# Performance work log

Measured on AMD Instinct MI355X. Metric: run time of the kernel, lower is better.

Reference implementation:

```python
import jax, jax.numpy as jnp
from jax import lax
import numpy as np

GB_MAX = 3      # BandEst guard-band upper bound
RB = 1          # refer_band
PAD = RB + 1    # refer_band + init_guard_band(1)
N_OFF = 16      # ring offsets: kernel (4,4) -> N=16
BN_EPS = 1e-5

def _ring_offsets():
    idx = np.arange(-PAD, PAD + 1)
    X, Y = np.meshgrid(idx, idx, indexing='ij')
    hp = wp = 2 * PAD + 1
    def ring(M):
        return np.concatenate([M[0:RB, 0:wp - RB].ravel(), M[0:hp - RB, wp - RB:wp].ravel(),
                               M[hp - RB:hp, RB:wp].ravel(), M[RB:hp, 0:RB].ravel()])
    return ring(X).astype(np.float32), ring(Y).astype(np.float32)

PRF_X, PRF_Y = _ring_offsets()
BLOCK = np.repeat(np.arange(4), N_OFF // 4)  # offset n -> direction block (top,right,bottom,left)


def q_shift(x, H, W, shift=1, gamma=0.25):
    B, T, C = x.shape
    img = x.transpose(0, 2, 1).reshape(B, C, H, W)
    g = int(C * gamma)
    out = jnp.zeros_like(img)
    out = out.at[:, 0:g, :, shift:].set(img[:, 0:g, :, :W - shift])
    out = out.at[:, g:2 * g, :, :W - shift].set(img[:, g:2 * g, :, shift:])
    out = out.at[:, 2 * g:3 * g, shift:, :].set(img[:, 2 * g:3 * g, :H - shift, :])
    out = out.at[:, 3 * g:4 * g, :H - shift, :].set(img[:, 3 * g:4 * g, shift:, :])
    out = out.at[:, 4 * g:].set(img[:, 4 * g:])
    return out.reshape(B, C, T).transpose(0, 2, 1)


def bi_wkv(w, u, k, v):
    # Bi-directional WKV: y_t = (sum_{i<t} e^{-(t-1-i)w + k_i} v_i + e^{u+k_t} v_t
    #                            + sum_{i>t} e^{-(i-1-t)w + k_i} v_i) / (same with v->1)
    B, T, C = k.shape
    kT = k.transpose(1, 0, 2)
    vT = v.transpose(1, 0, 2)

    def step(carry, kv):
        m, a, b = carry  # state represents e^m * (a, b): (sum exp, weighted v)
        kt, vt = kv
        out = (m, a, b)  # exclusive prefix (excludes current token)
        m2 = jnp.maximum(m - w, kt)
        e1 = jnp.exp(m - w - m2)
        e2 = jnp.exp(kt - m2)
        return (m2, e1 * a + e2, e1 * b + e2 * vt), out

    init = (jnp.full((B, C), -1e38, k.dtype), jnp.zeros((B, C), k.dtype), jnp.zeros((B, C), k.dtype))
    _, (mf, af, bf) = lax.scan(step, init, (kT, vT))
    _, (mb, ab, bb) = lax.scan(step, init, (kT[::-1], vT[::-1]))
    mb, ab, bb = mb[::-1], ab[::-1], bb[::-1]
    ms = u + kT
    M = jnp.maximum(jnp.maximum(mf, mb), ms)
    ef, eb, es = jnp.exp(mf - M), jnp.exp(mb - M), jnp.exp(ms - M)
    num = ef * bf + eb * bb + es * vT
    den = ef * af + eb * ab + es
    return (num / den).transpose(1, 0, 2)


def band_est(x, cvw, cvb, bns_v, bnb_v, chw, chb, bns_h, bnb_h):
    dn = ('NCHW', 'OIHW', 'NCHW')
    gv = lax.conv_general_dilated(x, cvw, (1, 1), ((GB_MAX, GB_MAX), (0, 0)), dimension_numbers=dn) + cvb[None, :, None, None]
    gh = lax.conv_general_dilated(x, chw, (1, 1), ((0, 0), (GB_MAX, GB_MAX)), dimension_numbers=dn) + chb[None, :, None, None]
    inv = np.float32(1.0 / np.sqrt(1.0 + BN_EPS))  # eval BN: running mean 0, var 1
    gv = gv * (bns_v * inv)[None, :, None, None] + bnb_v[None, :, None, None]
    gh = gh * (bns_h * inv)[None, :, None, None] + bnb_h[None, :, None, None]
    return jnp.concatenate([jax.nn.sigmoid(gv), jax.nn.sigmoid(gh)], 1) * (GB_MAX - 1)


def _gather(xp_flat, ix, iy, wp, h, w):
    b, c = xp_flat.shape[0], xp_flat.shape[1]
    idx = (ix * wp + iy).reshape(b, 1, -1)
    return jnp.take_along_axis(xp_flat, idx, axis=2).reshape(b, c, h, w, N_OFF)


def ada_peak(x_img, cvw, cvb, bns_v, bnb_v, chw, chb, bns_h, bnb_h):
    b, c, h, w = x_img.shape
    xp = jnp.pad(x_img, ((0, 0), (0, 0), (PAD, PAD), (PAD, PAD)), mode='edge')
    hp, wp = h + 2 * PAD, w + 2 * PAD
    xp_flat = xp.reshape(b, c, hp * wp)
    gb = band_est(x_img, cvw, cvb, bns_v, bnb_v, chw, chb, bns_h, bnb_h)  # (b,4,h,w)
    zero = jnp.zeros_like(gb[:, 0])
    mvx = jnp.stack([-gb[:, 0], zero, gb[:, 1], zero], -1)  # (b,h,w,4) per block
    mvy = jnp.stack([zero, gb[:, 3], zero, -gb[:, 2]], -1)
    move_x = mvx[..., BLOCK]  # (b,h,w,16)
    move_y = mvy[..., BLOCK]
    cx = jnp.arange(PAD, h + PAD, dtype=x_img.dtype)
    cy = jnp.arange(PAD, w + PAD, dtype=x_img.dtype)
    px = cx[None, :, None, None] + jnp.asarray(PRF_X)[None, None, None, :] + move_x
    py = cy[None, None, :, None] + jnp.asarray(PRF_Y)[None, None, None, :] + move_y
    flx = jnp.floor(lax.stop_gradient(px))
    fly = jnp.floor(lax.stop_gradient(py))
    q_lt_x = jnp.clip(flx, 0, hp - 1)
    q_lt_y = jnp.clip(fly, 0, wp - 1)
    q_rb_x = jnp.clip(flx + 1, 0, hp - 1)
    q_rb_y = jnp.clip(fly + 1, 0, wp - 1)
    pxc = jnp.clip(px, 0, hp - 1)
    pyc = jnp.clip(py, 0, wp - 1)
    g_lt = (1 + (q_lt_x - pxc)) * (1 + (q_lt_y - pyc))
    g_rb = (1 - (q_rb_x - pxc)) * (1 - (q_rb_y - pyc))
    x_lt = _gather(xp_flat, q_lt_x.astype(jnp.int32), q_lt_y.astype(jnp.int32), wp, h, w)
    x_rb = _gather(xp_flat, q_rb_x.astype(jnp.int32), q_rb_y.astype(jnp.int32), wp, h, w)
    x_r = g_lt[:, None] * x_lt + g_rb[:, None] * x_rb
    return x_img[..., None] - x_r  # (b,c,h,w,N): center-minus-reference peak feature


def setup_inputs():
    key = jax.random.key(0)
    B, H, W, C = 2, 64, 64, 192
    ks = jax.random.split(key, 16)
    s = 0.02
    return {
        'x': jax.random.normal(ks[0], (B, H * W, C), jnp.float32),
        'h': H, 'w': W,
        'mix_k': jax.random.uniform(ks[1], (1, 1, C), jnp.float32),
        'mix_v': jax.random.uniform(ks[2], (1, 1, C), jnp.float32),
        'mix_r': jax.random.uniform(ks[3], (1, 1, C), jnp.float32),
        'Wk': jax.random.normal(ks[4], (C, C), jnp.float32) * s,
        'Wv': jax.random.normal(ks[5], (C, C), jnp.float32) * s,
        'Wr': jax.random.normal(ks[6], (C, C), jnp.float32) * s,
        'Wo': jax.random.normal(ks[7], (C, C), jnp.float32) * s,
        'spatial_decay': jax.random.normal(ks[8], (C,), jnp.float32),
        'spatial_first': jax.random.normal(ks[9], (C,), jnp.float32),
        'cvw': jax.random.normal(ks[10], (2, C, 2 * GB_MAX + 1, 1), jnp.float32) * s,
        'cvb': jnp.zeros((2,), jnp.float32),
        'bns_v': jnp.ones((2,), jnp.float32),
        'bnb_v': jnp.zeros((2,), jnp.float32),
        'chw': jax.random.normal(ks[11], (2, C, 1, 2 * GB_MAX + 1), jnp.float32) * s,
        'chb': jnp.zeros((2,), jnp.float32),
        'bns_h': jnp.ones((2,), jnp.float32),
        'bnb_h': jnp.zeros((2,), jnp.float32),
    }


def reference(x, h, w, mix_k, mix_v, mix_r, Wk, Wv, Wr, Wo, spatial_decay, spatial_first,
              cvw, cvb, bns_v, bnb_v, chw, chb, bns_h, bnb_h):
    B, T, C = x.shape
    xx = q_shift(x, h, w)
    xk = x * mix_k + xx * (1 - mix_k)
    xv = x * mix_v + xx * (1 - mix_v)
    xr = x * mix_r + xx * (1 - mix_r)
    k = xk @ Wk
    v = xv @ Wv
    sr = jax.nn.sigmoid(xr @ Wr)
    # deformable peak branch (AdaPeak2D) on the token grid, pooled over the N=16 ring samples
    x_img = x.transpose(0, 2, 1).reshape(B, C, h, w)
    peak = ada_peak(x_img, cvw, cvb, bns_v, bnb_v, chw, chb, bns_h, bnb_h).mean(-1)
    v = v + peak.reshape(B, C, T).transpose(0, 2, 1)
    y = bi_wkv(spatial_decay / T, spatial_first / T, k, v)
    return (sr * y) @ Wo
```

## Files before the change

kernel.cpp:

```cpp
#include <hip/hip_runtime.h>
#include <hip/hip_bf16.h>

#define BATCH 2
#define TLEN 4096
#define CC 192
#define PADC 2

typedef __attribute__((ext_vector_type(8))) short bf16x8;
typedef __attribute__((ext_vector_type(4))) float f32x4;

__device__ __constant__ float PRF_X[16] = {-2,-2,-2,-2, -2,-1,0,1, 2,2,2,2, -1,0,1,2};
__device__ __constant__ float PRF_Y[16] = {-2,-1,0,1, 2,2,2,2, -1,0,1,2, -2,-2,-2,-2};

__device__ __forceinline__ unsigned short f2bf(float f) {
    unsigned u = __float_as_uint(f);
    u = (u + 0x7FFF + ((u >> 16) & 1)) >> 16;
    return (unsigned short)u;
}
__device__ __forceinline__ float bf2f(unsigned short h) {
    return __uint_as_float(((unsigned)h) << 16);
}

__global__ __launch_bounds__(256) void k_split_x(const float* __restrict__ x,
                                                 unsigned short* __restrict__ XH,
                                                 unsigned short* __restrict__ XL,
                                                 unsigned short* __restrict__ ZP) {
    if (blockIdx.x == 0 && threadIdx.x < 32) ZP[threadIdx.x] = 0;
    int idx = blockIdx.x * 256 + threadIdx.x;
    float4 v = *(const float4*)(x + (size_t)idx * 4);
    ushort4 hh, ll;
    float f, fh;
    f = v.x; hh.x = f2bf(f); fh = bf2f(hh.x); ll.x = f2bf(f - fh);
    f = v.y; hh.y = f2bf(f); fh = bf2f(hh.y); ll.y = f2bf(f - fh);
    f = v.z; hh.z = f2bf(f); fh = bf2f(hh.z); ll.z = f2bf(f - fh);
    f = v.w; hh.w = f2bf(f); fh = bf2f(hh.w); ll.w = f2bf(f - fh);
    *(ushort4*)(XH + (size_t)idx * 4) = hh;
    *(ushort4*)(XL + (size_t)idx * 4) = ll;
}

__global__ __launch_bounds__(256) void k_wcat_t(const float* __restrict__ Wk,
                                                const float* __restrict__ Wv,
                                                const float* __restrict__ Wr,
                                                const float* __restrict__ mk,
                                                const float* __restrict__ mv,
                                                const float* __restrict__ mr,
                                                unsigned short* __restrict__ WTH,
                                                unsigned short* __restrict__ WTL) {
    int idx = blockIdx.x * 256 + threadIdx.x;
    int n = idx / 384, k = idx - n * 384;
    int sec = n / CC, nc = n - sec * CC;
    const float* W   = (sec == 0) ? Wk : (sec == 1) ? Wv : Wr;
    const float* mix = (sec == 0) ? mk : (sec == 1) ? mv : mr;
    float wv = (k < CC) ? mix[k] * W[k * CC + nc]
                        : (1.0f - mix[k - CC]) * W[(k - CC) * CC + nc];
    unsigned short h = f2bf(wv);
    WTH[idx] = h;
    WTL[idx] = f2bf(wv - bf2f(h));
}

__global__ __launch_bounds__(256) void k_prep_wo(const float* __restrict__ Wo,
                                                 unsigned short* __restrict__ WoTH,
                                                 unsigned short* __restrict__ WoTL) {
    int idx = blockIdx.x * 256 + threadIdx.x;
    int n = idx / CC, k = idx - n * CC;
    float wv = Wo[k * CC + n];
    unsigned short h = f2bf(wv);
    WoTH[idx] = h;
    WoTL[idx] = f2bf(wv - bf2f(h));
}

__global__ __launch_bounds__(128, 2) void k_gemm1_mfma(
        const unsigned short* __restrict__ XH, const unsigned short* __restrict__ XL,
        const unsigned short* __restrict__ WTH, const unsigned short* __restrict__ WTL,
        const unsigned short* __restrict__ ZP,
        float* __restrict__ ZTk, float* __restrict__ Zv, float* __restrict__ ZTr) {
    __shared__ unsigned short sAh[128 * 32], sAl[128 * 32];
    __shared__ unsigned short sBh[64 * 32],  sBl[64 * 32];
    const int tid  = threadIdx.x;
    const int w    = tid >> 6;
    const int lane = tid & 63;
    const int bx = blockIdx.x;
    const int bm = blockIdx.y * 128;
    const int bn = bx * 64;

    const int lc  = tid & 3;
    const int ar0 = tid >> 2;

    f32x4 acc[4][4];
#pragma unroll
    for (int i = 0; i < 4; ++i)
#pragma unroll
        for (int j = 0; j < 4; ++j) acc[i][j] = f32x4{0.f, 0.f, 0.f, 0.f};

    uint4 rA[8], rB[4];

    auto loadA = [&](int step) {
        int k0 = step * 32;
#pragma unroll
        for (int q = 0; q < 4; ++q) {
            int rloc = ar0 + q * 32;
            int rg = bm + rloc;
            const unsigned short *srcH, *srcL;
            if (k0 < CC) {
                size_t o = (size_t)rg * CC + k0 + lc * 8;
                srcH = XH + o; srcL = XL + o;
            } else {
                int c = k0 - CC + lc * 8;
                int g = c / 48;
                int t = rg & (TLEN - 1);
                int ri = t >> 6, rj = t & 63;
                int dr; bool ok;
                if      (g == 0) { dr = -1;  ok = (rj > 0);  }
                else if (g == 1) { dr =  1;  ok = (rj < 63); }
                else if (g == 2) { dr = -64; ok = (ri > 0);  }
                else             { dr =  64; ok = (ri < 63); }
                if (ok) { size_t o = (size_t)(rg + dr) * CC + c; srcH = XH + o; srcL = XL + o; }
                else    { srcH = ZP; srcL = ZP; }
            }
            rA[q * 2]     = *(const uint4*)srcH;
            rA[q * 2 + 1] = *(const uint4*)srcL;
        }
    };
    auto loadB = [&](int step) {
        int k0 = step * 32;
#pragma unroll
        for (int q = 0; q < 2; ++q) {
            int col = ar0 + q * 32;
            size_t o = (size_t)(bn + col) * 384 + k0 + lc * 8;
            rB[q * 2]     = *(const uint4*)(WTH + o);
            rB[q * 2 + 1] = *(const uint4*)(WTL + o);
        }
    };
    auto writeS = [&]() {
#pragma unroll
        for (int q = 0; q < 4; ++q) {
            int off = (ar0 + q * 32) * 32 + lc * 8;
            *(uint4*)&sAh[off] = rA[q * 2];
            *(uint4*)&sAl[off] = rA[q * 2 + 1];
        }
#pragma unroll
        for (int q = 0; q < 2; ++q) {
            int off = (ar0 + q * 32) * 32 + lc * 8;
            *(uint4*)&sBh[off] = rB[q * 2];
            *(uint4*)&sBl[off] = rB[q * 2 + 1];
        }
    };

    const int r15 = lane & 15, ksub = lane >> 4;
    const int pc8 = ksub * 8;

    loadA(0); loadB(0);
    for (int step = 0; step < 12; ++step) {
        __syncthreads();
        writeS();
        __syncthreads();
        if (step < 11) { loadA(step + 1); loadB(step + 1); }
        bf16x8 ah[4], al[4], bh[4], bl[4];
#pragma unroll
        for (int f = 0; f < 4; ++f) {
            int ra = (w * 64 + f * 16 + r15) * 32 + pc8;
            ah[f] = *(const bf16x8*)&sAh[ra];
            al[f] = *(const bf16x8*)&sAl[ra];
            int rb = (f * 16 + r15) * 32 + pc8;
            bh[f] = *(const bf16x8*)&sBh[rb];
            bl[f] = *(const bf16x8*)&sBl[rb];
        }
#pragma unroll
        for (int fr = 0; fr < 4; ++fr)
#pragma unroll
            for (int fc = 0; fc < 4; ++fc) {
                acc[fr][fc] = __builtin_amdgcn_mfma_f32_16x16x32_bf16(ah[fr], bh[fc], acc[fr][fc], 0, 0, 0);
                acc[fr][fc] = __builtin_amdgcn_mfma_f32_16x16x32_bf16(ah[fr], bl[fc], acc[fr][fc], 0, 0, 0);
                acc[fr][fc] = __builtin_amdgcn_mfma_f32_16x16x32_bf16(al[fr], bh[fc], acc[fr][fc], 0, 0, 0);
            }
    }

    const int sec   = bx / 3;
    const int cbase = (bx - sec * 3) * 64;
#pragma unroll
    for (int fr = 0; fr < 4; ++fr) {
        int row0 = bm + w * 64 + fr * 16 + ksub * 4;
#pragma unroll
        for (int fc = 0; fc < 4; ++fc) {
            int col = cbase + fc * 16 + r15;
            f32x4 v = acc[fr][fc];
            if (sec == 1) {
#pragma unroll
                for (int rg = 0; rg < 4; ++rg)
                    Zv[(size_t)(row0 + rg) * CC + col] = v[rg];
            } else {
                float* D = (sec == 0) ? ZTk : ZTr;
                *(float4*)(D + (size_t)col * 8192 + row0) = make_float4(v[0], v[1], v[2], v[3]);
            }
        }
    }
}

__global__ __launch_bounds__(128, 2) void k_gemm2_mfma(
        const unsigned short* __restrict__ PH, const unsigned short* __restrict__ PL,
        const unsigned short* __restrict__ WoTH, const unsigned short* __restrict__ WoTL,
        float* __restrict__ out) {
    __shared__ unsigned short sAh[128 * 32], sAl[128 * 32];
    __shared__ unsigned short sBh[64 * 32],  sBl[64 * 32];
    const int tid  = threadIdx.x;
    const int w    = tid >> 6;
    const int lane = tid & 63;
    const int bn = blockIdx.x * 64;
    const int bm = blockIdx.y * 128;
    const int lc  = tid & 3;
    const int ar0 = tid >> 2;

    f32x4 acc[4][4];
#pragma unroll
    for (int i = 0; i < 4; ++i)
#pragma unroll
        for (int j = 0; j < 4; ++j) acc[i][j] = f32x4{0.f, 0.f, 0.f, 0.f};

    uint4 rA[8], rB[4];
    auto loadAB = [&](int step) {
        int k0 = step * 32;
#pragma unroll
        for (int q = 0; q < 4; ++q) {
            size_t o = (size_t)(bm + ar0 + q * 32) * CC + k0 + lc * 8;
            rA[q * 2]     = *(const uint4*)(PH + o);
            rA[q * 2 + 1] = *(const uint4*)(PL + o);
        }
#pragma unroll
        for (int q = 0; q < 2; ++q) {
            size_t o = (size_t)(bn + ar0 + q * 32) * CC + k0 + lc * 8;
            rB[q * 2]     = *(const uint4*)(WoTH + o);
            rB[q * 2 + 1] = *(const uint4*)(WoTL + o);
        }
    };
    auto writeS = [&]() {
#pragma unroll
        for (int q = 0; q < 4; ++q) {
            int off = (ar0 + q * 32) * 32 + lc * 8;
            *(uint4*)&sAh[off] = rA[q * 2];
            *(uint4*)&sAl[off] = rA[q * 2 + 1];
        }
#pragma unroll
        for (int q = 0; q < 2; ++q) {
            int off = (ar0 + q * 32) * 32 + lc * 8;
            *(uint4*)&sBh[off] = rB[q * 2];
            *(uint4*)&sBl[off] = rB[q * 2 + 1];
        }
    };

    const int r15 = lane & 15, ksub = lane >> 4;
    const int pc8 = ksub * 8;

    loadAB(0);
    for (int step = 0; step < 6; ++step) {
        __syncthreads();
        writeS();
        __syncthreads();
        if (step < 5) loadAB(step + 1);
        bf16x8 ah[4], al[4], bh[4], bl[4];
#pragma unroll
        for (int f = 0; f < 4; ++f) {
            int ra = (w * 64 + f * 16 + r15) * 32 + pc8;
            ah[f] = *(const bf16x8*)&sAh[ra];
            al[f] = *(const bf16x8*)&sAl[ra];
            int rb = (f * 16 + r15) * 32 + pc8;
            bh[f] = *(const bf16x8*)&sBh[rb];
            bl[f] = *(const bf16x8*)&sBl[rb];
        }
#pragma unroll
        for (int fr = 0; fr < 4; ++fr)
#pragma unroll
            for (int fc = 0; fc < 4; ++fc) {
                acc[fr][fc] = __builtin_amdgcn_mfma_f32_16x16x32_bf16(ah[fr], bh[fc], acc[fr][fc], 0, 0, 0);
                acc[fr][fc] = __builtin_amdgcn_mfma_f32_16x16x32_bf16(ah[fr], bl[fc], acc[fr][fc], 0, 0, 0);
                acc[fr][fc] = __builtin_amdgcn_mfma_f32_16x16x32_bf16(al[fr], bh[fc], acc[fr][fc], 0, 0, 0);
            }
    }

#pragma unroll
    for (int fr = 0; fr < 4; ++fr) {
        int row0 = bm + w * 64 + fr * 16 + ksub * 4;
#pragma unroll
        for (int fc = 0; fc < 4; ++fc) {
            int col = bn + fc * 16 + r15;
            f32x4 v = acc[fr][fc];
#pragma unroll
            for (int rg = 0; rg < 4; ++rg)
                out[(size_t)(row0 + rg) * CC + col] = v[rg];
        }
    }
}

__global__ __launch_bounds__(192) void k_bandpeak(const float* __restrict__ x,
                                                  const float* __restrict__ cvw,
                                                  const float* __restrict__ cvb,
                                                  const float* __restrict__ bns_v,
                                                  const float* __restrict__ bnb_v,
                                                  const float* __restrict__ chw,
                                                  const float* __restrict__ chb,
                                                  const float* __restrict__ bns_h,
                                                  const float* __restrict__ bnb_h,
                                                  float* __restrict__ Zv) {
    int pixg = blockIdx.x;
    int b   = pixg >> 12;
    int pix = pixg & 4095;
    int i = pix >> 6, j = pix & 63;
    int c = threadIdx.x;
    size_t xbase = (size_t)b * TLEN * CC;

    float sv0 = 0.f, sv1 = 0.f, sh0 = 0.f, sh1 = 0.f;
#pragma unroll
    for (int t = 0; t < 7; ++t) {
        int ii = i + t - 3;
        if (ii >= 0 && ii < 64) {
            float xv = x[xbase + (size_t)(ii * 64 + j) * CC + c];
            sv0 = fmaf(xv, cvw[(0 * CC + c) * 7 + t], sv0);
            sv1 = fmaf(xv, cvw[(1 * CC + c) * 7 + t], sv1);
        }
        int jj = j + t - 3;
        if (jj >= 0 && jj < 64) {
            float xh = x[xbase + (size_t)(i * 64 + jj) * CC + c];
            sh0 = fmaf(xh, chw[(0 * CC + c) * 7 + t], sh0);
            sh1 = fmaf(xh, chw[(1 * CC + c) * 7 + t], sh1);
        }
    }
    __shared__ float red[4][CC];
    __shared__ float gsh[4];
    red[0][c] = sv0; red[1][c] = sv1; red[2][c] = sh0; red[3][c] = sh1;
    __syncthreads();
    if (c < 64) {
#pragma unroll
        for (int r = 0; r < 4; ++r) {
            float v = red[r][c] + red[r][c + 64] + red[r][c + 128];
            v += __shfl_xor(v, 32);
            v += __shfl_xor(v, 16);
            v += __shfl_xor(v, 8);
            v += __shfl_xor(v, 4);
            v += __shfl_xor(v, 2);
            v += __shfl_xor(v, 1);
            if (c == 0) {
                const float inv = 0.9999950000374997f;
                float bias, sc, sh;
                if (r < 2) { bias = cvb[r];     sc = bns_v[r];     sh = bnb_v[r]; }
                else       { bias = chb[r - 2]; sc = bns_h[r - 2]; sh = bnb_h[r - 2]; }
                float g = (v + bias) * (sc * inv) + sh;
                gsh[r] = 2.0f / (1.0f + expf(-g));
            }
        }
    }
    __syncthreads();

    __shared__ int   l_lt[16], l_rb[16];
    __shared__ float l_glt[16], l_grb[16];
    if (c < 16) {
        int n = c, blk = n >> 2;
        float mx = (blk == 0) ? -gsh[0] : (blk == 2) ? gsh[1] : 0.0f;
        float my = (blk == 1) ?  gsh[3] : (blk == 3) ? -gsh[2] : 0.0f;
        float px = (float)(i + PADC) + PRF_X[n] + mx;
        float py = (float)(j + PADC) + PRF_Y[n] + my;
        float flx = floorf(px), fly = floorf(py);
        float qltx = fminf(fmaxf(flx, 0.f), 67.f);
        float qlty = fminf(fmaxf(fly, 0.f), 67.f);
        float qrbx = fminf(fmaxf(flx + 1.f, 0.f), 67.f);
        float qrby = fminf(fmaxf(fly + 1.f, 0.f), 67.f);
        float pxc = fminf(fmaxf(px, 0.f), 67.f);
        float pyc = fminf(fmaxf(py, 0.f), 67.f);
        float glt = (1.f + (qltx - pxc)) * (1.f + (qlty - pyc));
        float grb = (1.f - (qrbx - pxc)) * (1.f - (qrby - pyc));
        int sltx = min(max((int)qltx - PADC, 0), 63);
        int slty = min(max((int)qlty - PADC, 0), 63);
        int srbx = min(max((int)qrbx - PADC, 0), 63);
        int srby = min(max((int)qrby - PADC, 0), 63);
        l_lt[n] = sltx * 64 + slty;
        l_rb[n] = srbx * 64 + srby;
        l_glt[n] = glt;
        l_grb[n] = grb;
    }
    __syncthreads();

    float acc = 0.f;
#pragma unroll
    for (int n = 0; n < 16; ++n) {
        acc = fmaf(l_glt[n], x[xbase + (size_t)l_lt[n] * CC + c], acc);
        acc = fmaf(l_grb[n], x[xbase + (size_t)l_rb[n] * CC + c], acc);
    }
    float peak = x[xbase + (size_t)pix * CC + c] - acc * 0.0625f;
    Zv[((size_t)b * TLEN + pix) * CC + c] += peak;
}

__global__ __launch_bounds__(256) void k_transv(const float* __restrict__ Zv,
                                                float* __restrict__ ZTv) {
    __shared__ float tile[64][65];
    int tid = threadIdx.x;
    int rb = (blockIdx.x & 127) * 64;
    int cb = (blockIdx.x >> 7) * 64;
    int tr  = tid >> 4;
    int tc4 = (tid & 15) * 4;
#pragma unroll
    for (int q = 0; q < 4; ++q) {
        int r = tr + q * 16;
        float4 v = *(const float4*)(Zv + (size_t)(rb + r) * CC + cb + tc4);
        *(float4*)&tile[r][tc4] = v;
    }
    __syncthreads();
#pragma unroll
    for (int q = 0; q < 4; ++q) {
        int ccol = tr + q * 16;
        float4 o = {tile[tc4 + 0][ccol], tile[tc4 + 1][ccol],
                    tile[tc4 + 2][ccol], tile[tc4 + 3][ccol]};
        *(float4*)(ZTv + (size_t)(cb + ccol) * 8192 + rb + tc4) = o;
    }
}

__global__ __launch_bounds__(256) void k_transP(const float* __restrict__ PT,
                                                unsigned short* __restrict__ PH,
                                                unsigned short* __restrict__ PL) {
    __shared__ float tile[64][65];
    int tid = threadIdx.x;
    int mb = (blockIdx.x & 127) * 64;
    int cb = (blockIdx.x >> 7) * 64;
    int tr  = tid >> 4;
    int tc4 = (tid & 15) * 4;
#pragma unroll
    for (int q = 0; q < 4; ++q) {
        int cr = tr + q * 16;
        float4 v = *(const float4*)(PT + (size_t)(cb + cr) * 8192 + mb + tc4);
        *(float4*)&tile[cr][tc4] = v;
    }
    __syncthreads();
#pragma unroll
    for (int q = 0; q < 4; ++q) {
        int m = tr + q * 16;
        ushort4 hh, ll;
        float f, fh;
        f = tile[tc4 + 0][m]; hh.x = f2bf(f); fh = bf2f(hh.x); ll.x = f2bf(f - fh);
        f = tile[tc4 + 1][m]; hh.y = f2bf(f); fh = bf2f(hh.y); ll.y = f2bf(f - fh);
        f = tile[tc4 + 2][m]; hh.z = f2bf(f); fh = bf2f(hh.z); ll.z = f2bf(f - fh);
        f = tile[tc4 + 3][m]; hh.w = f2bf(f); fh = bf2f(hh.w); ll.w = f2bf(f - fh);
        size_t o = (size_t)(mb + m) * CC + cb + tc4;
        *(ushort4*)(PH + o) = hh;
        *(ushort4*)(PL + o) = ll;
    }
}

__global__ __launch_bounds__(256) void k_wkv2(const float* __restrict__ ZT,
                                              float* __restrict__ PT,
                                              const float* __restrict__ sd,
                                              const float* __restrict__ sf) {
    const int NTH = 256, CH = 16;
    int c = blockIdx.x % CC;
    int b = blockIdx.x / CC;
    const float w = sd[c] * (1.0f / 4096.0f);
    const float u = sf[c] * (1.0f / 4096.0f);

    __shared__ float s_m[NTH], s_a[NTH], s_b[NTH], s_L[NTH];

    int tid = threadIdx.x;
    int s = tid * CH;
    size_t rowbase = (size_t)b * TLEN;

    float kr[CH], vr[CH], rr[CH];
    {
        const float* pk = ZT + (size_t)c * 8192 + rowbase + s;
        const float* pv = ZT + (size_t)(CC + c) * 8192 + rowbase + s;
        const float* pr = ZT + (size_t)(2 * CC + c) * 8192 + rowbase + s;
#pragma unroll
        for (int q = 0; q < 4; ++q) {
            *(float4*)&kr[q * 4] = *(const float4*)(pk + q * 4);
            *(float4*)&vr[q * 4] = *(const float4*)(pv + q * 4);
            *(float4*)&rr[q * 4] = *(const float4*)(pr + q * 4);
        }
    }

    float m = -1e38f, a = 0.f, bb = 0.f;
#pragma unroll
    for (int jj = 0; jj < CH; ++jj) {
        float kt = kr[jj], vt = vr[jj];
        float m2 = fmaxf(m - w, kt);
        float e1 = expf(m - w - m2);
        float e2 = expf(kt - m2);
        a = e1 * a + e2;
        bb = e1 * bb + e2 * vt;
        m = m2;
    }
    s_m[tid] = m; s_a[tid] = a; s_b[tid] = bb; s_L[tid] = (float)CH;
    float L = (float)CH;
    for (int d = 1; d < NTH; d <<= 1) {
        __syncthreads();
        float pm = 0, pa = 0, pb = 0, pL = 0;
        bool has = (tid >= d);
        if (has) { pm = s_m[tid - d]; pa = s_a[tid - d]; pb = s_b[tid - d]; pL = s_L[tid - d]; }
        __syncthreads();
        if (has) {
            float pdec = pm - L * w;
            float m2 = fmaxf(pdec, m);
            float e1 = expf(pdec - m2);
            float e2 = expf(m - m2);
            a  = e1 * pa + e2 * a;
            bb = e1 * pb + e2 * bb;
            m = m2; L += pL;
            s_m[tid] = m; s_a[tid] = a; s_b[tid] = bb; s_L[tid] = L;
        }
    }
    __syncthreads();
    float fm = -1e38f, fa = 0.f, fb = 0.f;
    if (tid > 0) { fm = s_m[tid - 1]; fa = s_a[tid - 1]; fb = s_b[tid - 1]; }
    __syncthreads();

    m = -1e38f; a = 0.f; bb = 0.f;
#pragma unroll
    for (int jj = CH - 1; jj >= 0; --jj) {
        float kt = kr[jj], vt = vr[jj];
        float m2 = fmaxf(m - w, kt);
        float e1 = expf(m - w - m2);
        float e2 = expf(kt - m2);
        a = e1 * a + e2;
        bb = e1 * bb + e2 * vt;
        m = m2;
    }
    s_m[tid] = m; s_a[tid] = a; s_b[tid] = bb; s_L[tid] = (float)CH;
    L = (float)CH;
    for (int d = 1; d < NTH; d <<= 1) {
        __syncthreads();
        float pm = 0, pa = 0, pb = 0, pL = 0;
        bool has = (tid + d) < NTH;
        if (has) { pm = s_m[tid + d]; pa = s_a[tid + d]; pb = s_b[tid + d]; pL = s_L[tid + d]; }
        __syncthreads();
        if (has) {
            float pdec = pm - L * w;
            float m2 = fmaxf(m, pdec);
            float e1 = expf(m - m2);
            float e2 = expf(pdec - m2);
            a  = e1 * a + e2 * pa;
            bb = e1 * bb + e2 * pb;
            m = m2; L += pL;
            s_m[tid] = m; s_a[tid] = a; s_b[tid] = bb; s_L[tid] = L;
        }
    }
    __syncthreads();
    float bm = -1e38f, ba = 0.f, bbv = 0.f;
    if (tid < NTH - 1) { bm = s_m[tid + 1]; ba = s_a[tid + 1]; bbv = s_b[tid + 1]; }

    float em[CH], ea[CH], eb[CH];
    m = bm; a = ba; bb = bbv;
#pragma unroll
    for (int jj = CH - 1; jj >= 0; --jj) {
        em[jj] = m; ea[jj] = a; eb[jj] = bb;
        float kt = kr[jj], vt = vr[jj];
        float m2 = fmaxf(m - w, kt);
        float e1 = expf(m - w - m2);
        float e2 = expf(kt - m2);
        a = e1 * a + e2;
        bb = e1 * bb + e2 * vt;
        m = m2;
    }

    m = fm; a = fa; bb = fb;
#pragma unroll
    for (int jj = 0; jj < CH; ++jj) {
        float kt = kr[jj], vt = vr[jj];
        float ms = u + kt;
        float M = fmaxf(fmaxf(m, em[jj]), ms);
        float ef  = expf(m - M);
        float ebk = expf(em[jj] - M);
        float es  = expf(ms - M);
        float num = ef * bb + ebk * eb[jj] + es * vt;
        float den = ef * a + ebk * ea[jj] + es;
        float y = num / den;
        float sr = 1.0f / (1.0f + expf(-rr[jj]));
        PT[(size_t)c * 8192 + rowbase + s + jj] = sr * y;
        float m2 = fmaxf(m - w, kt);
        float e1 = expf(m - w - m2);
        float e2 = expf(kt - m2);
        a = e1 * a + e2;
        bb = e1 * bb + e2 * vt;
        m = m2;
    }
}

extern "C" void kernel_launch(void* const* d_in, const int* in_sizes, int n_in,
                              void* d_out, int out_size, void* d_ws, size_t ws_size,
                              hipStream_t stream) {
    const float* x     = (const float*)d_in[0];
    const float* mix_k = (const float*)d_in[3];
    const float* mix_v = (const float*)d_in[4];
    const float* mix_r = (const float*)d_in[5];
    const float* Wk    = (const float*)d_in[6];
    const float* Wv    = (const float*)d_in[7];
    const float* Wr    = (const float*)d_in[8];
    const float* Wo    = (const float*)d_in[9];
    const float* sd    = (const float*)d_in[10];
    const float* sf    = (const float*)d_in[11];
    const float* cvw   = (const float*)d_in[12];
    const float* cvb   = (const float*)d_in[13];
    const float* bns_v = (const float*)d_in[14];
    const float* bnb_v = (const float*)d_in[15];
    const float* chw   = (const float*)d_in[16];
    const float* chb   = (const float*)d_in[17];
    const float* bns_h = (const float*)d_in[18];
    const float* bnb_h = (const float*)d_in[19];
    float* out = (float*)d_out;
    char* W = (char*)d_ws;

    float*          Zv   = (float*)(W + 0);
    float*          ZTk  = (float*)(W + 6291456);
    float*          ZTv  = (float*)(W + 12582912);
    float*          ZTr  = (float*)(W + 18874368);
    unsigned short* XH   = (unsigned short*)(W + 12582912);
    unsigned short* XL   = (unsigned short*)(W + 15728640);
    unsigned short* PH   = (unsigned short*)(W + 6291456);
    unsigned short* PL   = (unsigned short*)(W + 9437184);
    float*          PT   = Zv;
    unsigned short* WTH  = (unsigned short*)(W + 25165824);
    unsigned short* WTL  = (unsigned short*)(W + 25608192);
    unsigned short* WoTH = (unsigned short*)(W + 26050560);
    unsigned short* WoTL = (unsigned short*)(W + 26124288);
    unsigned short* ZP   = (unsigned short*)(W + 26198016);

    k_split_x<<<1536, 256, 0, stream>>>(x, XH, XL, ZP);
    k_wcat_t<<<864, 256, 0, stream>>>(Wk, Wv, Wr, mix_k, mix_v, mix_r, WTH, WTL);
    k_prep_wo<<<144, 256, 0, stream>>>(Wo, WoTH, WoTL);
    k_gemm1_mfma<<<dim3(9, 64), 128, 0, stream>>>(XH, XL, WTH, WTL, ZP, ZTk, Zv, ZTr);
    k_bandpeak<<<8192, 192, 0, stream>>>(x, cvw, cvb, bns_v, bnb_v, chw, chb, bns_h, bnb_h, Zv);
    k_transv<<<384, 256, 0, stream>>>(Zv, ZTv);
    k_wkv2<<<384, 256, 0, stream>>>(ZTk, PT, sd, sf);
    k_transP<<<384, 256, 0, stream>>>(PT, PH, PL);
    k_gemm2_mfma<<<dim3(3, 64), 128, 0, stream>>>(PH, PL, WoTH, WoTL, out);
}
```

Measured before the change: 264.4 us.

## Pad GEMM LDS tiles, stage epilogues through LDS, coalesce WKV loads/stores

After: 264.7 us. About the same (+0.1%).

```diff
diff --git a/kernel.cpp b/kernel.cpp
--- a/kernel.cpp
+++ b/kernel.cpp
@@ -5,6 +5,8 @@
 #define TLEN 4096
 #define CC 192
 #define PADC 2
+#define APAD 40
+#define WPAD 265
 
 typedef __attribute__((ext_vector_type(8))) short bf16x8;
 typedef __attribute__((ext_vector_type(4))) float f32x4;
@@ -74,15 +76,18 @@
         const unsigned short* __restrict__ WTH, const unsigned short* __restrict__ WTL,
         const unsigned short* __restrict__ ZP,
         float* __restrict__ ZTk, float* __restrict__ Zv, float* __restrict__ ZTr) {
-    __shared__ unsigned short sAh[128 * 32], sAl[128 * 32];
-    __shared__ unsigned short sBh[64 * 32],  sBl[64 * 32];
+    __shared__ __align__(16) char smem[34816];
+    unsigned short* sAh = (unsigned short*)(smem);
+    unsigned short* sAl = (unsigned short*)(smem + 10240);
+    unsigned short* sBh = (unsigned short*)(smem + 20480);
+    unsigned short* sBl = (unsigned short*)(smem + 25600);
+
     const int tid  = threadIdx.x;
     const int w    = tid >> 6;
     const int lane = tid & 63;
     const int bx = blockIdx.x;
     const int bm = blockIdx.y * 128;
     const int bn = bx * 64;
-
     const int lc  = tid & 3;
     const int ar0 = tid >> 2;
 
@@ -98,8 +103,7 @@
         int k0 = step * 32;
 #pragma unroll
         for (int q = 0; q < 4; ++q) {
-            int rloc = ar0 + q * 32;
-            int rg = bm + rloc;
+            int rg = bm + ar0 + q * 32;
             const unsigned short *srcH, *srcL;
             if (k0 < CC) {
                 size_t o = (size_t)rg * CC + k0 + lc * 8;
@@ -125,8 +129,7 @@
         int k0 = step * 32;
 #pragma unroll
         for (int q = 0; q < 2; ++q) {
-            int col = ar0 + q * 32;
-            size_t o = (size_t)(bn + col) * 384 + k0 + lc * 8;
+            size_t o = (size_t)(bn + ar0 + q * 32) * 384 + k0 + lc * 8;
             rB[q * 2]     = *(const uint4*)(WTH + o);
             rB[q * 2 + 1] = *(const uint4*)(WTL + o);
         }
@@ -134,13 +137,13 @@
     auto writeS = [&]() {
 #pragma unroll
         for (int q = 0; q < 4; ++q) {
-            int off = (ar0 + q * 32) * 32 + lc * 8;
+            int off = (ar0 + q * 32) * APAD + lc * 8;
             *(uint4*)&sAh[off] = rA[q * 2];
             *(uint4*)&sAl[off] = rA[q * 2 + 1];
         }
 #pragma unroll
         for (int q = 0; q < 2; ++q) {
-            int off = (ar0 + q * 32) * 32 + lc * 8;
+            int off = (ar0 + q * 32) * APAD + lc * 8;
             *(uint4*)&sBh[off] = rB[q * 2];
             *(uint4*)&sBl[off] = rB[q * 2 + 1];
         }
@@ -158,10 +161,10 @@
         bf16x8 ah[4], al[4], bh[4], bl[4];
 #pragma unroll
         for (int f = 0; f < 4; ++f) {
-            int ra = (w * 64 + f * 16 + r15) * 32 + pc8;
+            int ra = (w * 64 + f * 16 + r15) * APAD + pc8;
             ah[f] = *(const bf16x8*)&sAh[ra];
             al[f] = *(const bf16x8*)&sAl[ra];
-            int rb = (f * 16 + r15) * 32 + pc8;
+            int rb = (f * 16 + r15) * APAD + pc8;
             bh[f] = *(const bf16x8*)&sBh[rb];
             bl[f] = *(const bf16x8*)&sBl[rb];
         }
@@ -175,23 +178,45 @@
             }
     }
 
+    __syncthreads();
+    float* T = (float*)smem + w * (64 * 68);
     const int sec   = bx / 3;
     const int cbase = (bx - sec * 3) * 64;
-#pragma unroll
-    for (int fr = 0; fr < 4; ++fr) {
-        int row0 = bm + w * 64 + fr * 16 + ksub * 4;
-#pragma unroll
-        for (int fc = 0; fc < 4; ++fc) {
-            int col = cbase + fc * 16 + r15;
-            f32x4 v = acc[fr][fc];
-            if (sec == 1) {
-#pragma unroll
-                for (int rg = 0; rg < 4; ++rg)
-                    Zv[(size_t)(row0 + rg) * CC + col] = v[rg];
-            } else {
-                float* D = (sec == 0) ? ZTk : ZTr;
-                *(float4*)(D + (size_t)col * 8192 + row0) = make_float4(v[0], v[1], v[2], v[3]);
+
+    if (sec == 1) {
+#pragma unroll
+        for (int fr = 0; fr < 4; ++fr)
+#pragma unroll
+            for (int fc = 0; fc < 4; ++fc) {
+                int r0 = fr * 16 + ksub * 4, c = fc * 16 + r15;
+                f32x4 v = acc[fr][fc];
+                T[(r0 + 0) * 68 + c] = v[0];
+                T[(r0 + 1) * 68 + c] = v[1];
+                T[(r0 + 2) * 68 + c] = v[2];
+                T[(r0 + 3) * 68 + c] = v[3];
             }
+        __syncthreads();
+#pragma unroll
+        for (int it = 0; it < 16; ++it) {
+            int row = it * 4 + ksub;
+            float4 o = *(const float4*)&T[row * 68 + r15 * 4];
+            *(float4*)(Zv + (size_t)(bm + w * 64 + row) * CC + cbase + r15 * 4) = o;
+        }
+    } else {
+        float* D = (sec == 0) ? ZTk : ZTr;
+#pragma unroll
+        for (int fr = 0; fr < 4; ++fr)
+#pragma unroll
+            for (int fc = 0; fc < 4; ++fc) {
+                int r0 = fr * 16 + ksub * 4, c = fc * 16 + r15;
+                *(f32x4*)&T[c * 68 + r0] = acc[fr][fc];
+            }
+        __syncthreads();
+#pragma unroll
+        for (int cg = 0; cg < 16; ++cg) {
+            int c = cg * 4 + ksub;
+            float4 o = *(const float4*)&T[c * 68 + r15 * 4];
+            *(float4*)(D + (size_t)(cbase + c) * 8192 + bm + w * 64 + r15 * 4) = o;
         }
     }
 }
@@ -200,8 +225,12 @@
         const unsigned short* __restrict__ PH, const unsigned short* __restrict__ PL,
         const unsigned short* __restrict__ WoTH, const unsigned short* __restrict__ WoTL,
         float* __restrict__ out) {
-    __shared__ unsigned short sAh[128 * 32], sAl[128 * 32];
-    __shared__ unsigned short sBh[64 * 32],  sBl[64 * 32];
+    __shared__ __align__(16) char smem[34816];
+    unsigned short* sAh = (unsigned short*)(smem);
+    unsigned short* sAl = (unsigned short*)(smem + 10240);
+    unsigned short* sBh = (unsigned short*)(smem + 20480);
+    unsigned short* sBl = (unsigned short*)(smem + 25600);
+
     const int tid  = threadIdx.x;
     const int w    = tid >> 6;
     const int lane = tid & 63;
@@ -235,13 +264,13 @@
     auto writeS = [&]() {
 #pragma unroll
         for (int q = 0; q < 4; ++q) {
-            int off = (ar0 + q * 32) * 32 + lc * 8;
+            int off = (ar0 + q * 32) * APAD + lc * 8;
             *(uint4*)&sAh[off] = rA[q * 2];
             *(uint4*)&sAl[off] = rA[q * 2 + 1];
         }
 #pragma unroll
         for (int q = 0; q < 2; ++q) {
-            int off = (ar0 + q * 32) * 32 + lc * 8;
+            int off = (ar0 + q * 32) * APAD + lc * 8;
             *(uint4*)&sBh[off] = rB[q * 2];
             *(uint4*)&sBl[off] = rB[q * 2 + 1];
         }
@@ -259,10 +288,10 @@
         bf16x8 ah[4], al[4], bh[4], bl[4];
 #pragma unroll
         for (int f = 0; f < 4; ++f) {
-            int ra = (w * 64 + f * 16 + r15) * 32 + pc8;
+            int ra = (w * 64 + f * 16 + r15) * APAD + pc8;
             ah[f] = *(const bf16x8*)&sAh[ra];
             al[f] = *(const bf16x8*)&sAl[ra];
-            int rb = (f * 16 + r15) * 32 + pc8;
+            int rb = (f * 16 + r15) * APAD + pc8;
             bh[f] = *(const bf16x8*)&sBh[rb];
             bl[f] = *(const bf16x8*)&sBl[rb];
         }
@@ -276,17 +305,25 @@
             }
     }
 
-#pragma unroll
-    for (int fr = 0; fr < 4; ++fr) {
-        int row0 = bm + w * 64 + fr * 16 + ksub * 4;
+    __syncthreads();
+    float* T = (float*)smem + w * (64 * 68);
+#pragma unroll
+    for (int fr = 0; fr < 4; ++fr)
 #pragma unroll
         for (int fc = 0; fc < 4; ++fc) {
-            int col = bn + fc * 16 + r15;
+            int r0 = fr * 16 + ksub * 4, c = fc * 16 + r15;
             f32x4 v = acc[fr][fc];
-#pragma unroll
-            for (int rg = 0; rg < 4; ++rg)
-                out[(size_t)(row0 + rg) * CC + col] = v[rg];
-        }
+            T[(r0 + 0) * 68 + c] = v[0];
+            T[(r0 + 1) * 68 + c] = v[1];
+            T[(r0 + 2) * 68 + c] = v[2];
+            T[(r0 + 3) * 68 + c] = v[3];
+        }
+    __syncthreads();
+#pragma unroll
+    for (int it = 0; it < 16; ++it) {
+        int row = it * 4 + ksub;
+        float4 o = *(const float4*)&T[row * 68 + r15 * 4];
+        *(float4*)(out + (size_t)(bm + w * 64 + row) * CC + bn + r15 * 4) = o;
     }
 }
 
@@ -452,24 +489,38 @@
     const float w = sd[c] * (1.0f / 4096.0f);
     const float u = sf[c] * (1.0f / 4096.0f);
 
+    __shared__ float buf[16 * WPAD];
     __shared__ float s_m[NTH], s_a[NTH], s_b[NTH], s_L[NTH];
 
     int tid = threadIdx.x;
-    int s = tid * CH;
-    size_t rowbase = (size_t)b * TLEN;
+    size_t base = (size_t)c * 8192 + (size_t)b * TLEN;
 
     float kr[CH], vr[CH], rr[CH];
-    {
-        const float* pk = ZT + (size_t)c * 8192 + rowbase + s;
-        const float* pv = ZT + (size_t)(CC + c) * 8192 + rowbase + s;
-        const float* pr = ZT + (size_t)(2 * CC + c) * 8192 + rowbase + s;
-#pragma unroll
-        for (int q = 0; q < 4; ++q) {
-            *(float4*)&kr[q * 4] = *(const float4*)(pk + q * 4);
-            *(float4*)&vr[q * 4] = *(const float4*)(pv + q * 4);
-            *(float4*)&rr[q * 4] = *(const float4*)(pr + q * 4);
-        }
-    }
+
+    auto coopLoad = [&](const float* src) {
+#pragma unroll
+        for (int i = 0; i < 4; ++i) {
+            int g = i * 1024 + tid * 4;
+            float4 v = *(const float4*)(src + g);
+            int jj0 = g & 15;
+            int tp  = g >> 4;
+            buf[(jj0 + 0) * WPAD + tp] = v.x;
+            buf[(jj0 + 1) * WPAD + tp] = v.y;
+            buf[(jj0 + 2) * WPAD + tp] = v.z;
+            buf[(jj0 + 3) * WPAD + tp] = v.w;
+        }
+    };
+    auto chunkRead = [&](float* dst) {
+#pragma unroll
+        for (int jj = 0; jj < CH; ++jj) dst[jj] = buf[jj * WPAD + tid];
+    };
+
+    coopLoad(ZT + base);                                __syncthreads();
+    chunkRead(kr);                                      __syncthreads();
+    coopLoad(ZT + (size_t)CC * 8192 + base);            __syncthreads();
+    chunkRead(vr);                                      __syncthreads();
+    coopLoad(ZT + (size_t)2 * CC * 8192 + base);        __syncthreads();
+    chunkRead(rr);                                      __syncthreads();
 
     float m = -1e38f, a = 0.f, bb = 0.f;
 #pragma unroll
@@ -539,6 +590,7 @@
     __syncthreads();
     float bm = -1e38f, ba = 0.f, bbv = 0.f;
     if (tid < NTH - 1) { bm = s_m[tid + 1]; ba = s_a[tid + 1]; bbv = s_b[tid + 1]; }
+    __syncthreads();
 
     float em[CH], ea[CH], eb[CH];
     m = bm; a = ba; bb = bbv;
@@ -567,13 +619,23 @@
         float den = ef * a + ebk * ea[jj] + es;
         float y = num / den;
         float sr = 1.0f / (1.0f + expf(-rr[jj]));
-        PT[(size_t)c * 8192 + rowbase + s + jj] = sr * y;
+        buf[jj * WPAD + tid] = sr * y;
         float m2 = fmaxf(m - w, kt);
         float e1 = expf(m - w - m2);
         float e2 = expf(kt - m2);
         a = e1 * a + e2;
         bb = e1 * bb + e2 * vt;
         m = m2;
+    }
+    __syncthreads();
+#pragma unroll
+    for (int i = 0; i < 4; ++i) {
+        int g = i * 1024 + tid * 4;
+        int jj0 = g & 15;
+        int tp  = g >> 4;
+        float4 o = {buf[(jj0 + 0) * WPAD + tp], buf[(jj0 + 1) * WPAD + tp],
+                    buf[(jj0 + 2) * WPAD + tp], buf[(jj0 + 3) * WPAD + tp]};
+        *(float4*)(PT + base + g) = o;
     }
 }
 
```
